# Kernel optimization log

Hardware: AMD Instinct MI355X
Metric: run time of the kernel (lower is better)

Reference implementation:

```python
import jax, jax.numpy as jnp
import numpy as np

B, DIMS = 8192, 1024
FCN = [DIMS, 2048, 1024, 512, 1]   # self.fcn_dims = [dims] + fcn_dims + [1]
C = 8                               # cluster_num
NLAYERS = len(FCN) - 1              # layer_num = 4


def setup_inputs() -> dict:
    key = jax.random.key(0)
    ks = jax.random.split(key, 2 + 2 * NLAYERS)
    inp = {}
    inp["x"] = jax.random.normal(ks[0], (B, DIMS), dtype=jnp.float32)
    # cluster centers, L2-normalized rows (as in __init__)
    c = jax.random.normal(ks[1], (C, DIMS), dtype=jnp.float32)
    inp["center"] = c / jnp.linalg.norm(c, axis=1, keepdims=True)
    for i in range(NLAYERS):
        fan_in, fan_out = FCN[i], FCN[i + 1]
        # xavier_uniform with relu gain
        gain = float(np.sqrt(2.0))
        bound = gain * float(np.sqrt(6.0 / (fan_in + fan_out)))
        inp[f"w0_{i}"] = jax.random.uniform(ks[2 + 2 * i], (fan_in, fan_out), jnp.float32, -bound, bound)
        inp[f"wc_{i}"] = jax.random.uniform(ks[3 + 2 * i], (C, fan_in, fan_out), jnp.float32, -bound, bound)
    return inp


def _forward(x, center, w0s, wcs):
    # --- router (eval mode: single pass, no center update, no grad) ---
    xd = jax.lax.stop_gradient(x)
    sij = xd @ jax.lax.stop_gradient(center).T          # [B, C]
    router = jnp.argmax(sij, axis=1)                     # [B]
    # --- all cluster towers, gated weights w0 * w_d ---
    h = jnp.broadcast_to(x[None], (C,) + x.shape)        # [C, B, dims]
    for i in range(NLAYERS - 1):
        w = w0s[i][None] * wcs[i]                        # [C, in, out]
        h = jax.nn.relu(jnp.einsum('cbi,cio->cbo', h, w))
    w = w0s[-1][None] * wcs[-1]                          # [C, in, 1]
    h = jax.nn.sigmoid(jnp.einsum('cbi,cio->cbo', h, w))  # [C, B, 1]
    out = jnp.transpose(h[:, :, 0])                      # [B, C]
    # gather per-sample selected cluster output
    return jnp.take_along_axis(out, router[:, None], axis=1)[:, 0]  # [B]


def reference(x, center, w0_0, w0_1, w0_2, w0_3, wc_0, wc_1, wc_2, wc_3):
    w0s = [w0_0, w0_1, w0_2, w0_3]
    wcs = [wc_0, wc_1, wc_2, wc_3]
    return _forward(x, center, w0s, wcs)
```

## Files before the change

### kernel.cpp

```cpp
#include <hip/hip_runtime.h>
#include <hip/hip_bf16.h>

#define B_SZ 8192
#define DIMS 1024
#define CLN 8
#define BM 128
#define PADMAX (B_SZ + CLN * BM)
#define MAX_TILES (B_SZ / BM + CLN)

typedef __attribute__((ext_vector_type(8))) __bf16 bf16x8;
typedef __attribute__((ext_vector_type(8))) short short8;
typedef __attribute__((ext_vector_type(4))) short short4v;
typedef __attribute__((ext_vector_type(4))) float f32x4;

__device__ __forceinline__ short f2bf(float f) {
  __hip_bfloat16 h = __float2bfloat16(f);
  return __builtin_bit_cast(short, h);
}
__device__ __forceinline__ float bf2f(short s) {
  unsigned u = ((unsigned)(unsigned short)s) << 16;
  return __builtin_bit_cast(float, u);
}

__device__ __forceinline__ void gl_lds16(const void* g, void* l) {
  __builtin_amdgcn_global_load_lds(
      (const __attribute__((address_space(1))) unsigned int*)(unsigned long long)(uintptr_t)g,
      (__attribute__((address_space(3))) unsigned int*)(unsigned long long)(uintptr_t)l,
      16, 0, 0);
}

__device__ __forceinline__ void router_body(const float* __restrict__ x,
                                            const float* __restrict__ center,
                                            int* __restrict__ router, short* __restrict__ xb,
                                            int bx) {
  const int tid = threadIdx.x;
  const int lane = tid & 63;
  const int w = tid >> 6;
  const int s = bx * 4 + w;
  const float4* xr = (const float4*)(x + (size_t)s * DIMS);
  float4 xv[4];
#pragma unroll
  for (int j = 0; j < 4; ++j) xv[j] = xr[j * 64 + lane];
  if (xb) {
    short* xbr = xb + (size_t)s * DIMS;
#pragma unroll
    for (int j = 0; j < 4; ++j) {
      short4v sv;
      sv[0] = f2bf(xv[j].x); sv[1] = f2bf(xv[j].y);
      sv[2] = f2bf(xv[j].z); sv[3] = f2bf(xv[j].w);
      *(short4v*)(xbr + j * 256 + lane * 4) = sv;
    }
  }
  float p[CLN];
#pragma unroll
  for (int c = 0; c < CLN; ++c) p[c] = 0.f;
#pragma unroll
  for (int j = 0; j < 4; ++j) {
    float4 cv[CLN];
#pragma unroll
    for (int c = 0; c < CLN; ++c)
      cv[c] = ((const float4*)(center + (size_t)c * DIMS))[j * 64 + lane];
#pragma unroll
    for (int c = 0; c < CLN; ++c)
      p[c] += xv[j].x * cv[c].x + xv[j].y * cv[c].y + xv[j].z * cv[c].z + xv[j].w * cv[c].w;
  }
#pragma unroll
  for (int c = 0; c < CLN; ++c) {
#pragma unroll
    for (int m = 1; m < 64; m <<= 1) p[c] += __shfl_xor(p[c], m);
  }
  if (lane == 0) {
    int best = 0; float bv = p[0];
#pragma unroll
    for (int c = 1; c < CLN; ++c) { if (p[c] > bv) { bv = p[c]; best = c; } }
    router[s] = best;
  }
}

template <int K, int N>
__device__ __forceinline__ void gate_body(const float* __restrict__ w0,
                                          const float* __restrict__ wc,
                                          short* __restrict__ gwt, int bx,
                                          float* ldsA, float* ldsB) {
  constexpr int KB = K / 64, NB = N / 64;
  const int c = bx / (KB * NB);
  const int rem = bx % (KB * NB);
  const int k0 = (rem / NB) * 64;
  const int n0 = (rem % NB) * 64;
  const int tid = threadIdx.x;
  const int lane = tid & 63;
  const int w = tid >> 6;
  const int rrow = lane >> 4;
  const int rseg = lane & 15;
  const float* wcp = wc + (size_t)c * K * N;
#pragma unroll
  for (int j = 0; j < 4; ++j) {
    const int chunk = j * 4 + w;
    const size_t goff = (size_t)(k0 + chunk * 4 + rrow) * N + n0 + rseg * 4;
    gl_lds16(w0 + goff, ldsA + chunk * 256);
    gl_lds16(wcp + goff, ldsB + chunk * 256);
  }
  __syncthreads();
  const int n = tid >> 2;
  const int seg = tid & 3;
  short8 o0, o1;
#pragma unroll
  for (int u = 0; u < 8; ++u) {
    const int k = seg * 16 + u;
    o0[u] = f2bf(ldsA[k * 64 + n] * ldsB[k * 64 + n]);
  }
#pragma unroll
  for (int u = 0; u < 8; ++u) {
    const int k = seg * 16 + 8 + u;
    o1[u] = f2bf(ldsA[k * 64 + n] * ldsB[k * 64 + n]);
  }
  short* dst = gwt + ((size_t)c * N + n0 + n) * K + k0 + seg * 16;
  *(short8*)dst = o0;
  *(short8*)(dst + 8) = o1;
}

__global__ void __launch_bounds__(256, 4)
prep_kernel(const float* __restrict__ x, const float* __restrict__ center,
            int* __restrict__ router, short* __restrict__ xb,
            const float* w00, const float* wc0, short* g0,
            const float* w01, const float* wc1, short* g1,
            const float* w02, const float* wc2, short* g2) {
  __shared__ float ldsA[64 * 64];
  __shared__ float ldsB[64 * 64];
  const int bx = blockIdx.x;
  if (bx < 2048) { router_body(x, center, router, xb, bx); return; }
  const int gx = bx - 2048;
  if (gx < 4096)       gate_body<1024, 2048>(w00, wc0, g0, gx, ldsA, ldsB);
  else if (gx < 8192)  gate_body<2048, 1024>(w01, wc1, g1, gx - 4096, ldsA, ldsB);
  else                 gate_body<1024, 512>(w02, wc2, g2, gx - 8192, ldsA, ldsB);
}

__global__ void __launch_bounds__(256, 4)
router_kernel(const float* __restrict__ x, const float* __restrict__ center,
              int* __restrict__ router, short* __restrict__ xb) {
  router_body(x, center, router, xb, blockIdx.x);
}

template <int K, int N>
__global__ void __launch_bounds__(256, 4)
gate1_kernel(const float* __restrict__ w0, const float* __restrict__ wc,
             short* __restrict__ gwt) {
  __shared__ float ldsA[64 * 64];
  __shared__ float ldsB[64 * 64];
  gate_body<K, N>(w0, wc, gwt, blockIdx.x, ldsA, ldsB);
}

__global__ void sort_kernel(const int* __restrict__ router, int* __restrict__ counts,
                            int* __restrict__ pstart, int* __restrict__ meta,
                            int* __restrict__ tile_c, int* __restrict__ tile_r,
                            int* __restrict__ order, float* __restrict__ z) {
  __shared__ int bins[CLN];
  __shared__ int cur[CLN];
  __shared__ int ps_s[CLN + 1];
  const int t = threadIdx.x;
  const int lane = t & 63;
  for (int p = t; p < PADMAX; p += 1024) z[p] = 0.f;
  if (t < CLN) bins[t] = 0;
  __syncthreads();
  int myc[8];
#pragma unroll
  for (int j = 0; j < 8; ++j) myc[j] = router[t + 1024 * j];
#pragma unroll
  for (int j = 0; j < 8; ++j) {
#pragma unroll
    for (int c = 0; c < CLN; ++c) {
      unsigned long long m = __ballot(myc[j] == c);
      if (lane == 0 && m) atomicAdd(&bins[c], __popcll(m));
    }
  }
  __syncthreads();
  if (t == 0) {
    int ps = 0, nt = 0;
    for (int c = 0; c < CLN; ++c) {
      const int tot = bins[c];
      counts[c] = tot; pstart[c] = ps; ps_s[c] = ps; cur[c] = 0;
      const int tiles = (tot + BM - 1) / BM;
      for (int i = 0; i < tiles; ++i) { tile_c[nt] = c; tile_r[nt] = ps + i * BM; ++nt; }
      ps += tiles * BM;
    }
    pstart[CLN] = ps; ps_s[CLN] = ps; meta[0] = nt; meta[1] = ps;
  }
  __syncthreads();
#pragma unroll
  for (int j = 0; j < 8; ++j) {
    const int s = t + 1024 * j;
    const int c = myc[j];
    int pos = 0;
#pragma unroll
    for (int cc = 0; cc < CLN; ++cc) {
      unsigned long long m = __ballot(c == cc);
      int b = 0;
      if (lane == 0 && m) b = atomicAdd(&cur[cc], __popcll(m));
      b = __shfl(b, 0);
      if (c == cc) pos = ps_s[cc] + b + __popcll(m & ((1ull << lane) - 1ull));
    }
    order[pos] = s;
  }
  __syncthreads();
  for (int p = t; p < PADMAX; p += 1024) {
#pragma unroll
    for (int c = 0; c < CLN; ++c) {
      if (p >= ps_s[c] && p < ps_s[c + 1]) {
        if (p - ps_s[c] >= bins[c]) order[p] = order[ps_s[c]];
        break;
      }
    }
  }
}

template <int K, int N, bool GATHER, bool FUSE_DOT>
__global__ void gemm_async(const short* __restrict__ Abase, const short* __restrict__ gwt,
                           short* __restrict__ Aout, const int* __restrict__ order,
                           const int* __restrict__ tile_c, const int* __restrict__ tile_r,
                           const int* __restrict__ meta,
                           const float* __restrict__ w03, const float* __restrict__ wc3,
                           float* __restrict__ z) {
  constexpr int NT = N / 128;
  const int bt = blockIdx.x / NT;
  if (bt >= meta[0]) return;
  const int n0 = (blockIdx.x % NT) * 128;
  const int cl = tile_c[bt];
  const int row0 = tile_r[bt];

  __shared__ __align__(16) short As[128 * 32];
  __shared__ __align__(16) short Bs[128 * 32];

  const int tid = threadIdx.x;
  const int lane = tid & 63;
  const int w = tid >> 6;
  const int wm = w >> 1;
  const int wn = w & 1;

  const int lrow = lane >> 2;
  const int kofs = (lane & 3) << 3;
  const short* ga0;
  const short* ga1;
  if (GATHER) {
    ga0 = Abase + (size_t)order[row0 + w * 16 + lrow] * K + kofs;
    ga1 = Abase + (size_t)order[row0 + 64 + w * 16 + lrow] * K + kofs;
  } else {
    ga0 = Abase + (size_t)(row0 + w * 16 + lrow) * K + kofs;
    ga1 = ga0 + (size_t)64 * K;
  }
  const short* gb0 = gwt + ((size_t)cl * N + n0 + w * 16 + lrow) * K + kofs;
  const short* gb1 = gb0 + (size_t)64 * K;
  short* lA0 = &As[w * 16 * 32];
  short* lA1 = &As[(64 + w * 16) * 32];
  short* lB0 = &Bs[w * 16 * 32];
  short* lB1 = &Bs[(64 + w * 16) * 32];

  f32x4 acc[4][4] = {};
  const int arL = wm * 64 + (lane & 15);
  const int bcL = wn * 64 + (lane & 15);
  const int kq = (lane >> 4) << 3;

  for (int kb = 0; kb < K; kb += 32) {
    __syncthreads();
    gl_lds16(ga0 + kb, lA0);
    gl_lds16(ga1 + kb, lA1);
    gl_lds16(gb0 + kb, lB0);
    gl_lds16(gb1 + kb, lB1);
    __syncthreads();

    short8 af[4], bfr[4];
#pragma unroll
    for (int mi = 0; mi < 4; ++mi) af[mi] = *(const short8*)&As[(arL + mi * 16) * 32 + kq];
#pragma unroll
    for (int ni = 0; ni < 4; ++ni) bfr[ni] = *(const short8*)&Bs[(bcL + ni * 16) * 32 + kq];
#pragma unroll
    for (int mi = 0; mi < 4; ++mi) {
#pragma unroll
      for (int ni = 0; ni < 4; ++ni) {
        acc[mi][ni] = __builtin_amdgcn_mfma_f32_16x16x32_bf16(
            __builtin_bit_cast(bf16x8, af[mi]), __builtin_bit_cast(bf16x8, bfr[ni]),
            acc[mi][ni], 0, 0, 0);
      }
    }
  }

  const int er = (lane >> 4) << 2;
  const int ec = lane & 15;
  if constexpr (FUSE_DOT) {
    float g[4];
#pragma unroll
    for (int ni = 0; ni < 4; ++ni) {
      const int col = n0 + wn * 64 + ni * 16 + ec;
      g[ni] = w03[col] * wc3[cl * N + col];
    }
#pragma unroll
    for (int mi = 0; mi < 4; ++mi) {
#pragma unroll
      for (int r = 0; r < 4; ++r) {
        float v = 0.f;
#pragma unroll
        for (int ni = 0; ni < 4; ++ni) v += fmaxf(acc[mi][ni][r], 0.f) * g[ni];
#pragma unroll
        for (int m = 1; m < 16; m <<= 1) v += __shfl_xor(v, m);
        if ((lane & 15) == 0)
          atomicAdd(&z[row0 + wm * 64 + mi * 16 + er + r], v);
      }
    }
  } else {
#pragma unroll
    for (int mi = 0; mi < 4; ++mi) {
#pragma unroll
      for (int ni = 0; ni < 4; ++ni) {
#pragma unroll
        for (int r = 0; r < 4; ++r) {
          float vv = fmaxf(acc[mi][ni][r], 0.f);
          const int row = row0 + wm * 64 + mi * 16 + er + r;
          const int col = n0 + wn * 64 + ni * 16 + ec;
          Aout[(size_t)row * N + col] = f2bf(vv);
        }
      }
    }
  }
}

__global__ void final_kernel(const float* __restrict__ z, const int* __restrict__ order,
                             const int* __restrict__ meta, float* __restrict__ out) {
  const int r = blockIdx.x * 256 + threadIdx.x;
  if (r < meta[1]) out[order[r]] = 1.f / (1.f + expf(-z[r]));
}

template <int K, int N, bool GATHER>
__global__ void gemm_layer(const float* __restrict__ Xf, const short* __restrict__ Ain,
                           const float* __restrict__ w0, const float* __restrict__ wc,
                           short* __restrict__ Aout,
                           const int* __restrict__ order,
                           const int* __restrict__ tile_c, const int* __restrict__ tile_r,
                           const int* __restrict__ meta) {
  const int bt = blockIdx.x;
  if (bt >= meta[0]) return;
  const int cl = tile_c[bt];
  const int row0 = tile_r[bt];
  const int n0 = blockIdx.y * 128;

  __shared__ __align__(16) short As[128 * 40];
  __shared__ __align__(16) short Bs[128 * 40];

  const int tid = threadIdx.x;
  const int lane = tid & 63;
  const int wm = (tid >> 6) >> 1;
  const int wn = (tid >> 6) & 1;

  f32x4 acc[4][4] = {};

  const int arow = tid >> 2;
  const int akseg = (tid & 3) << 3;
  const int bn = tid & 127;
  const int bkq = (tid >> 7) << 3;

  const float* xr0 = nullptr; const float* xr1 = nullptr;
  const short* ar0 = nullptr; const short* ar1 = nullptr;
  if (GATHER) {
    xr0 = Xf + (size_t)order[row0 + arow] * K + akseg;
    xr1 = Xf + (size_t)order[row0 + arow + 64] * K + akseg;
  } else {
    ar0 = Ain + (size_t)(row0 + arow) * K + akseg;
    ar1 = Ain + (size_t)(row0 + arow + 64) * K + akseg;
  }
  const float* w0p = w0 + n0 + bn;
  const float* wcp = wc + (size_t)cl * K * N + n0 + bn;

  for (int kb = 0; kb < K; kb += 32) {
    __syncthreads();
    if (GATHER) {
      float4 a = *(const float4*)(xr0 + kb);
      float4 b = *(const float4*)(xr0 + kb + 4);
      short8 v;
      v[0] = f2bf(a.x); v[1] = f2bf(a.y); v[2] = f2bf(a.z); v[3] = f2bf(a.w);
      v[4] = f2bf(b.x); v[5] = f2bf(b.y); v[6] = f2bf(b.z); v[7] = f2bf(b.w);
      *(short8*)&As[arow * 40 + akseg] = v;
      a = *(const float4*)(xr1 + kb);
      b = *(const float4*)(xr1 + kb + 4);
      v[0] = f2bf(a.x); v[1] = f2bf(a.y); v[2] = f2bf(a.z); v[3] = f2bf(a.w);
      v[4] = f2bf(b.x); v[5] = f2bf(b.y); v[6] = f2bf(b.z); v[7] = f2bf(b.w);
      *(short8*)&As[(arow + 64) * 40 + akseg] = v;
    } else {
      *(short8*)&As[arow * 40 + akseg] = *(const short8*)(ar0 + kb);
      *(short8*)&As[(arow + 64) * 40 + akseg] = *(const short8*)(ar1 + kb);
    }
#pragma unroll
    for (int half = 0; half < 2; ++half) {
      const int kk = bkq + half * 16;
      short8 v;
#pragma unroll
      for (int j = 0; j < 8; ++j) {
        const size_t off = (size_t)(kb + kk + j) * N;
        v[j] = f2bf(w0p[off] * wcp[off]);
      }
      *(short8*)&Bs[bn * 40 + kk] = v;
    }
    __syncthreads();

    const int arL = wm * 64 + (lane & 15);
    const int kq = (lane >> 4) << 3;
    const int bcL = wn * 64 + (lane & 15);
    short8 af[4], bfr[4];
#pragma unroll
    for (int mi = 0; mi < 4; ++mi) af[mi] = *(const short8*)&As[(arL + mi * 16) * 40 + kq];
#pragma unroll
    for (int ni = 0; ni < 4; ++ni) bfr[ni] = *(const short8*)&Bs[(bcL + ni * 16) * 40 + kq];
#pragma unroll
    for (int mi = 0; mi < 4; ++mi) {
#pragma unroll
      for (int ni = 0; ni < 4; ++ni) {
        acc[mi][ni] = __builtin_amdgcn_mfma_f32_16x16x32_bf16(
            __builtin_bit_cast(bf16x8, af[mi]), __builtin_bit_cast(bf16x8, bfr[ni]),
            acc[mi][ni], 0, 0, 0);
      }
    }
  }

  const int er = (lane >> 4) << 2;
  const int ec = lane & 15;
#pragma unroll
  for (int mi = 0; mi < 4; ++mi) {
#pragma unroll
    for (int ni = 0; ni < 4; ++ni) {
#pragma unroll
      for (int r = 0; r < 4; ++r) {
        float vv = fmaxf(acc[mi][ni][r], 0.f);
        const int row = row0 + wm * 64 + mi * 16 + er + r;
        const int col = n0 + wn * 64 + ni * 16 + ec;
        Aout[(size_t)row * N + col] = f2bf(vv);
      }
    }
  }
}

__global__ void layer3_kernel(const short* __restrict__ h2, const float* __restrict__ w03,
                              const float* __restrict__ wc3, const int* __restrict__ order,
                              const int* __restrict__ pstart, const int* __restrict__ meta,
                              float* __restrict__ out) {
  const int tid = threadIdx.x;
  const int lane = tid & 63;
  const int w = tid >> 6;
  const int r = blockIdx.x * 4 + w;
  if (r >= meta[1]) return;
  int c = 0;
#pragma unroll
  for (int i = 1; i < CLN; ++i) { if (r >= pstart[i]) c = i; }
  const short* hr = h2 + (size_t)r * 512;
  const int k0 = lane * 8;
  const short8 hv = *(const short8*)(hr + k0);
  const float* wcr = wc3 + c * 512;
  float part = 0.f;
#pragma unroll
  for (int j = 0; j < 8; ++j) part += bf2f(hv[j]) * w03[k0 + j] * wcr[k0 + j];
  for (int off = 32; off; off >>= 1) part += __shfl_down(part, off);
  if (lane == 0) out[order[r]] = 1.f / (1.f + expf(-part));
}

extern "C" void kernel_launch(void* const* d_in, const int* in_sizes, int n_in,
                              void* d_out, int out_size, void* d_ws, size_t ws_size,
                              hipStream_t stream) {
  const float* x = (const float*)d_in[0];
  const float* center = (const float*)d_in[1];
  const float* w0s[4]; const float* wcs[4];
  if (in_sizes[3] == 8 * in_sizes[2]) {
    for (int i = 0; i < 4; ++i) { w0s[i] = (const float*)d_in[2 + 2 * i]; wcs[i] = (const float*)d_in[3 + 2 * i]; }
  } else {
    for (int i = 0; i < 4; ++i) { w0s[i] = (const float*)d_in[2 + i]; wcs[i] = (const float*)d_in[6 + i]; }
  }
  float* out = (float*)d_out;
  char* ws = (char*)d_ws;
  int* counts = (int*)(ws + 0);
  int* pstart = (int*)(ws + 128);
  int* meta   = (int*)(ws + 192);
  int* tile_c = (int*)(ws + 256);
  int* tile_r = (int*)(ws + 1024);
  int* router = (int*)(ws + 4096);
  int* order  = (int*)(ws + 4096 + 4 * B_SZ);
  float* z    = (float*)(ws + 4096 + 4 * B_SZ + 4 * PADMAX);

  const size_t GW0 = (size_t)CLN * 1024 * 2048 * 2;
  const size_t GW1 = (size_t)CLN * 2048 * 1024 * 2;
  const size_t GW2 = (size_t)CLN * 1024 * 512 * 2;
  const size_t H0B = (size_t)PADMAX * 2048 * 2;
  const size_t H1B = (size_t)PADMAX * 1024 * 2;
  const size_t NEED_A = 131072 + GW0 + GW1 + GW2 + H0B + H1B;
  const size_t NEED_B = 131072 + GW1 + H0B + H1B;
  const int tier = (ws_size >= NEED_A) ? 0 : (ws_size >= NEED_B) ? 1 : 2;

  if (tier == 0) {
    short* gw0 = (short*)(ws + 131072);
    short* gw1 = (short*)(ws + 131072 + GW0);
    short* gw2 = (short*)(ws + 131072 + GW0 + GW1);
    short* h0  = (short*)(ws + 131072 + GW0 + GW1 + GW2);
    short* h1  = (short*)(ws + 131072 + GW0 + GW1 + GW2 + H0B);
    short* xb  = h1;

    prep_kernel<<<2048 + 9216, 256, 0, stream>>>(x, center, router, xb,
                                                 w0s[0], wcs[0], gw0,
                                                 w0s[1], wcs[1], gw1,
                                                 w0s[2], wcs[2], gw2);
    sort_kernel<<<1, 1024, 0, stream>>>(router, counts, pstart, meta, tile_c, tile_r, order, z);
    gemm_async<1024, 2048, true, false><<<MAX_TILES * 16, 256, 0, stream>>>(
        xb, gw0, h0, order, tile_c, tile_r, meta, nullptr, nullptr, nullptr);
    gemm_async<2048, 1024, false, false><<<MAX_TILES * 8, 256, 0, stream>>>(
        h0, gw1, h1, order, tile_c, tile_r, meta, nullptr, nullptr, nullptr);
    gemm_async<1024, 512, false, true><<<MAX_TILES * 4, 256, 0, stream>>>(
        h1, gw2, nullptr, order, tile_c, tile_r, meta, w0s[3], wcs[3], z);
    final_kernel<<<PADMAX / 256, 256, 0, stream>>>(z, order, meta, out);
  } else if (tier == 1) {
    short* gw = (short*)(ws + 131072);
    short* h0 = (short*)(ws + 131072 + GW1);
    short* h1 = (short*)(ws + 131072 + GW1 + H0B);
    short* xb = h1;

    router_kernel<<<2048, 256, 0, stream>>>(x, center, router, xb);
    sort_kernel<<<1, 1024, 0, stream>>>(router, counts, pstart, meta, tile_c, tile_r, order, z);
    gate1_kernel<1024, 2048><<<4096, 256, 0, stream>>>(w0s[0], wcs[0], gw);
    gemm_async<1024, 2048, true, false><<<MAX_TILES * 16, 256, 0, stream>>>(
        xb, gw, h0, order, tile_c, tile_r, meta, nullptr, nullptr, nullptr);
    gate1_kernel<2048, 1024><<<4096, 256, 0, stream>>>(w0s[1], wcs[1], gw);
    gemm_async<2048, 1024, false, false><<<MAX_TILES * 8, 256, 0, stream>>>(
        h0, gw, h1, order, tile_c, tile_r, meta, nullptr, nullptr, nullptr);
    gate1_kernel<1024, 512><<<1024, 256, 0, stream>>>(w0s[2], wcs[2], gw);
    gemm_async<1024, 512, false, true><<<MAX_TILES * 4, 256, 0, stream>>>(
        h1, gw, nullptr, order, tile_c, tile_r, meta, w0s[3], wcs[3], z);
    final_kernel<<<PADMAX / 256, 256, 0, stream>>>(z, order, meta, out);
  } else {
    short* f0 = (short*)(ws + 131072);
    short* f1 = f0 + (size_t)PADMAX * 2048;
    short* f2 = f1 + (size_t)PADMAX * 1024;
    router_kernel<<<2048, 256, 0, stream>>>(x, center, router, nullptr);
    sort_kernel<<<1, 1024, 0, stream>>>(router, counts, pstart, meta, tile_c, tile_r, order, z);
    gemm_layer<1024, 2048, true><<<dim3(MAX_TILES, 16), 256, 0, stream>>>(
        x, nullptr, w0s[0], wcs[0], f0, order, tile_c, tile_r, meta);
    gemm_layer<2048, 1024, false><<<dim3(MAX_TILES, 8), 256, 0, stream>>>(
        nullptr, f0, w0s[1], wcs[1], f1, order, tile_c, tile_r, meta);
    gemm_layer<1024, 512, false><<<dim3(MAX_TILES, 4), 256, 0, stream>>>(
        nullptr, f1, w0s[2], wcs[2], f2, order, tile_c, tile_r, meta);
    layer3_kernel<<<(PADMAX + 3) / 4, 256, 0, stream>>>(f2, w0s[3], wcs[3], order, pstart, meta, out);
  }
}
```

Baseline: 396.9 us.

## Fuse weight gating into GEMM tiles instead of precomputing gated bf16 weights

Removes the separate prep/gate kernels that materialized w0*wc as transposed bf16 weight tensors. Each GEMM block now loads fp32 w0 and wc tiles into LDS, multiplies and converts them to bf16 into a padded B tile, then runs MFMA. This avoids writing and rereading the gated weight buffers and reduces workspace needs. The cost is redundant gating across M-tiles of each cluster, double-width fp32 weight loads, an extra barrier per k-step, and larger LDS usage.

Measured after the change: 528.8 us. 33.2% more time.

```diff
diff --git a/kernel.cpp b/kernel.cpp
--- a/kernel.cpp
+++ b/kernel.cpp
@@ -29,10 +29,10 @@
       16, 0, 0);
 }
 
-__device__ __forceinline__ void router_body(const float* __restrict__ x,
-                                            const float* __restrict__ center,
-                                            int* __restrict__ router, short* __restrict__ xb,
-                                            int bx) {
+__global__ void __launch_bounds__(256, 4)
+router_kernel(const float* __restrict__ x, const float* __restrict__ center,
+              int* __restrict__ router, short* __restrict__ xb) {
+  const int bx = blockIdx.x;
   const int tid = threadIdx.x;
   const int lane = tid & 63;
   const int w = tid >> 6;
@@ -75,79 +75,6 @@
     for (int c = 1; c < CLN; ++c) { if (p[c] > bv) { bv = p[c]; best = c; } }
     router[s] = best;
   }
-}
-
-template <int K, int N>
-__device__ __forceinline__ void gate_body(const float* __restrict__ w0,
-                                          const float* __restrict__ wc,
-                                          short* __restrict__ gwt, int bx,
-                                          float* ldsA, float* ldsB) {
-  constexpr int KB = K / 64, NB = N / 64;
-  const int c = bx / (KB * NB);
-  const int rem = bx % (KB * NB);
-  const int k0 = (rem / NB) * 64;
-  const int n0 = (rem % NB) * 64;
-  const int tid = threadIdx.x;
-  const int lane = tid & 63;
-  const int w = tid >> 6;
-  const int rrow = lane >> 4;
-  const int rseg = lane & 15;
-  const float* wcp = wc + (size_t)c * K * N;
-#pragma unroll
-  for (int j = 0; j < 4; ++j) {
-    const int chunk = j * 4 + w;
-    const size_t goff = (size_t)(k0 + chunk * 4 + rrow) * N + n0 + rseg * 4;
-    gl_lds16(w0 + goff, ldsA + chunk * 256);
-    gl_lds16(wcp + goff, ldsB + chunk * 256);
-  }
-  __syncthreads();
-  const int n = tid >> 2;
-  const int seg = tid & 3;
-  short8 o0, o1;
-#pragma unroll
-  for (int u = 0; u < 8; ++u) {
-    const int k = seg * 16 + u;
-    o0[u] = f2bf(ldsA[k * 64 + n] * ldsB[k * 64 + n]);
-  }
-#pragma unroll
-  for (int u = 0; u < 8; ++u) {
-    const int k = seg * 16 + 8 + u;
-    o1[u] = f2bf(ldsA[k * 64 + n] * ldsB[k * 64 + n]);
-  }
-  short* dst = gwt + ((size_t)c * N + n0 + n) * K + k0 + seg * 16;
-  *(short8*)dst = o0;
-  *(short8*)(dst + 8) = o1;
-}
-
-__global__ void __launch_bounds__(256, 4)
-prep_kernel(const float* __restrict__ x, const float* __restrict__ center,
-            int* __restrict__ router, short* __restrict__ xb,
-            const float* w00, const float* wc0, short* g0,
-            const float* w01, const float* wc1, short* g1,
-            const float* w02, const float* wc2, short* g2) {
-  __shared__ float ldsA[64 * 64];
-  __shared__ float ldsB[64 * 64];
-  const int bx = blockIdx.x;
-  if (bx < 2048) { router_body(x, center, router, xb, bx); return; }
-  const int gx = bx - 2048;
-  if (gx < 4096)       gate_body<1024, 2048>(w00, wc0, g0, gx, ldsA, ldsB);
-  else if (gx < 8192)  gate_body<2048, 1024>(w01, wc1, g1, gx - 4096, ldsA, ldsB);
-  else                 gate_body<1024, 512>(w02, wc2, g2, gx - 8192, ldsA, ldsB);
-}
-
-__global__ void __launch_bounds__(256, 4)
-router_kernel(const float* __restrict__ x, const float* __restrict__ center,
-              int* __restrict__ router, short* __restrict__ xb) {
-  router_body(x, center, router, xb, blockIdx.x);
-}
-
-template <int K, int N>
-__global__ void __launch_bounds__(256, 4)
-gate1_kernel(const float* __restrict__ w0, const float* __restrict__ wc,
-             short* __restrict__ gwt) {
-  __shared__ float ldsA[64 * 64];
-  __shared__ float ldsB[64 * 64];
-  gate_body<K, N>(w0, wc, gwt, blockIdx.x, ldsA, ldsB);
 }
 
 __global__ void sort_kernel(const int* __restrict__ router, int* __restrict__ counts,
@@ -214,7 +141,8 @@
 }
 
 template <int K, int N, bool GATHER, bool FUSE_DOT>
-__global__ void gemm_async(const short* __restrict__ Abase, const short* __restrict__ gwt,
+__global__ void gemm_fused(const short* __restrict__ Abase,
+                           const float* __restrict__ w0g, const float* __restrict__ wcg,
                            short* __restrict__ Aout, const int* __restrict__ order,
                            const int* __restrict__ tile_c, const int* __restrict__ tile_r,
                            const int* __restrict__ meta,
@@ -228,7 +156,9 @@
   const int row0 = tile_r[bt];
 
   __shared__ __align__(16) short As[128 * 32];
-  __shared__ __align__(16) short Bs[128 * 32];
+  __shared__ __align__(16) short Bs[128 * 40];
+  __shared__ __align__(16) float Fw[32 * 128];
+  __shared__ __align__(16) float Fc[32 * 128];
 
   const int tid = threadIdx.x;
   const int lane = tid & 63;
@@ -247,12 +177,16 @@
     ga0 = Abase + (size_t)(row0 + w * 16 + lrow) * K + kofs;
     ga1 = ga0 + (size_t)64 * K;
   }
-  const short* gb0 = gwt + ((size_t)cl * N + n0 + w * 16 + lrow) * K + kofs;
-  const short* gb1 = gb0 + (size_t)64 * K;
   short* lA0 = &As[w * 16 * 32];
   short* lA1 = &As[(64 + w * 16) * 32];
-  short* lB0 = &Bs[w * 16 * 32];
-  short* lB1 = &Bs[(64 + w * 16) * 32];
+
+  const int brow = lane >> 5;
+  const int bcol = (lane & 31) * 4;
+  const float* gw = w0g + n0 + bcol;
+  const float* gc = wcg + (size_t)cl * K * N + n0 + bcol;
+
+  const int n2 = (tid & 63) * 2;
+  const int kh = (tid >> 6) * 8;
 
   f32x4 acc[4][4] = {};
   const int arL = wm * 64 + (lane & 15);
@@ -263,15 +197,31 @@
     __syncthreads();
     gl_lds16(ga0 + kb, lA0);
     gl_lds16(ga1 + kb, lA1);
-    gl_lds16(gb0 + kb, lB0);
-    gl_lds16(gb1 + kb, lB1);
+#pragma unroll
+    for (int j = 0; j < 4; ++j) {
+      const int r2 = w * 8 + j * 2;
+      const size_t go = (size_t)(kb + r2 + brow) * N;
+      gl_lds16(gw + go, &Fw[r2 * 128]);
+      gl_lds16(gc + go, &Fc[r2 * 128]);
+    }
     __syncthreads();
+    short8 o0, o1;
+#pragma unroll
+    for (int dk = 0; dk < 8; ++dk) {
+      const float2 a = *(const float2*)&Fw[(kh + dk) * 128 + n2];
+      const float2 b = *(const float2*)&Fc[(kh + dk) * 128 + n2];
+      o0[dk] = f2bf(a.x * b.x);
+      o1[dk] = f2bf(a.y * b.y);
+    }
+    *(short8*)&Bs[n2 * 40 + kh] = o0;
+    *(short8*)&Bs[(n2 + 1) * 40 + kh] = o1;
+    __syncthreads();
 
     short8 af[4], bfr[4];
 #pragma unroll
     for (int mi = 0; mi < 4; ++mi) af[mi] = *(const short8*)&As[(arL + mi * 16) * 32 + kq];
 #pragma unroll
-    for (int ni = 0; ni < 4; ++ni) bfr[ni] = *(const short8*)&Bs[(bcL + ni * 16) * 32 + kq];
+    for (int ni = 0; ni < 4; ++ni) bfr[ni] = *(const short8*)&Bs[(bcL + ni * 16) * 40 + kq];
 #pragma unroll
     for (int mi = 0; mi < 4; ++mi) {
 #pragma unroll
@@ -480,52 +430,23 @@
   int* order  = (int*)(ws + 4096 + 4 * B_SZ);
   float* z    = (float*)(ws + 4096 + 4 * B_SZ + 4 * PADMAX);
 
-  const size_t GW0 = (size_t)CLN * 1024 * 2048 * 2;
-  const size_t GW1 = (size_t)CLN * 2048 * 1024 * 2;
-  const size_t GW2 = (size_t)CLN * 1024 * 512 * 2;
   const size_t H0B = (size_t)PADMAX * 2048 * 2;
   const size_t H1B = (size_t)PADMAX * 1024 * 2;
-  const size_t NEED_A = 131072 + GW0 + GW1 + GW2 + H0B + H1B;
-  const size_t NEED_B = 131072 + GW1 + H0B + H1B;
-  const int tier = (ws_size >= NEED_A) ? 0 : (ws_size >= NEED_B) ? 1 : 2;
-
-  if (tier == 0) {
-    short* gw0 = (short*)(ws + 131072);
-    short* gw1 = (short*)(ws + 131072 + GW0);
-    short* gw2 = (short*)(ws + 131072 + GW0 + GW1);
-    short* h0  = (short*)(ws + 131072 + GW0 + GW1 + GW2);
-    short* h1  = (short*)(ws + 131072 + GW0 + GW1 + GW2 + H0B);
-    short* xb  = h1;
-
-    prep_kernel<<<2048 + 9216, 256, 0, stream>>>(x, center, router, xb,
-                                                 w0s[0], wcs[0], gw0,
-                                                 w0s[1], wcs[1], gw1,
-                                                 w0s[2], wcs[2], gw2);
-    sort_kernel<<<1, 1024, 0, stream>>>(router, counts, pstart, meta, tile_c, tile_r, order, z);
-    gemm_async<1024, 2048, true, false><<<MAX_TILES * 16, 256, 0, stream>>>(
-        xb, gw0, h0, order, tile_c, tile_r, meta, nullptr, nullptr, nullptr);
-    gemm_async<2048, 1024, false, false><<<MAX_TILES * 8, 256, 0, stream>>>(
-        h0, gw1, h1, order, tile_c, tile_r, meta, nullptr, nullptr, nullptr);
-    gemm_async<1024, 512, false, true><<<MAX_TILES * 4, 256, 0, stream>>>(
-        h1, gw2, nullptr, order, tile_c, tile_r, meta, w0s[3], wcs[3], z);
-    final_kernel<<<PADMAX / 256, 256, 0, stream>>>(z, order, meta, out);
-  } else if (tier == 1) {
-    short* gw = (short*)(ws + 131072);
-    short* h0 = (short*)(ws + 131072 + GW1);
-    short* h1 = (short*)(ws + 131072 + GW1 + H0B);
+  const size_t NEED_F = 131072 + H0B + H1B;
+
+  if (ws_size >= NEED_F) {
+    short* h0 = (short*)(ws + 131072);
+    short* h1 = (short*)(ws + 131072 + H0B);
     short* xb = h1;
 
     router_kernel<<<2048, 256, 0, stream>>>(x, center, router, xb);
     sort_kernel<<<1, 1024, 0, stream>>>(router, counts, pstart, meta, tile_c, tile_r, order, z);
-    gate1_kernel<1024, 2048><<<4096, 256, 0, stream>>>(w0s[0], wcs[0], gw);
-    gemm_async<1024, 2048, true, false><<<MAX_TILES * 16, 256, 0, stream>>>(
-        xb, gw, h0, order, tile_c, tile_r, meta, nullptr, nullptr, nullptr);
-    gate1_kernel<2048, 1024><<<4096, 256, 0, stream>>>(w0s[1], wcs[1], gw);
-    gemm_async<2048, 1024, false, false><<<MAX_TILES * 8, 256, 0, stream>>>(
-        h0, gw, h1, order, tile_c, tile_r, meta, nullptr, nullptr, nullptr);
-    gate1_kernel<1024, 512><<<1024, 256, 0, stream>>>(w0s[2], wcs[2], gw);
-    gemm_async<1024, 512, false, true><<<MAX_TILES * 4, 256, 0, stream>>>(
-        h1, gw, nullptr, order, tile_c, tile_r, meta, w0s[3], wcs[3], z);
+    gemm_fused<1024, 2048, true, false><<<MAX_TILES * 16, 256, 0, stream>>>(
+        xb, w0s[0], wcs[0], h0, order, tile_c, tile_r, meta, nullptr, nullptr, nullptr);
+    gemm_fused<2048, 1024, false, false><<<MAX_TILES * 8, 256, 0, stream>>>(
+        h0, w0s[1], wcs[1], h1, order, tile_c, tile_r, meta, nullptr, nullptr, nullptr);
+    gemm_fused<1024, 512, false, true><<<MAX_TILES * 4, 256, 0, stream>>>(
+        h1, w0s[2], wcs[2], nullptr, order, tile_c, tile_r, meta, w0s[3], wcs[3], z);
     final_kernel<<<PADMAX / 256, 256, 0, stream>>>(z, order, meta, out);
   } else {
     short* f0 = (short*)(ws + 131072);
```
